# Kernel tuning notes

Hardware: AMD Instinct MI355X
Metric: run time of the kernel (lower is better)

The kernel has to match this reference:

```python
import jax, jax.numpy as jnp
import numpy as np

VAR_NUM = 96
EMBED_TIME = 128
INPUT_DIM = VAR_NUM * 2 + EMBED_TIME  # 320
ATTN_DIM = 64
N_HEADS = 8
ALL_DIM = ATTN_DIM * N_HEADS  # 512
B, N = 8, 2048
NEG_INF = -1e9  # finite stand-in for masked_fill(-inf); safe under softmax


def setup_inputs() -> dict:
    key = jax.random.key(0)
    ks = jax.random.split(key, 16)
    s = lambda d: 1.0 / np.sqrt(d)
    return {
        "times_in": jax.random.uniform(ks[0], (B, N), jnp.float32),
        "data_in": jax.random.normal(ks[1], (B, N, VAR_NUM), jnp.float32),
        "mask_in": jnp.ones((B, N, VAR_NUM), jnp.float32),
        "exist_times": jax.random.randint(ks[2], (B, N), 0, 2, jnp.int32),
        # TimeEmbedding params
        "w_per": jax.random.normal(ks[3], (1, EMBED_TIME - 1), jnp.float32),
        "b_per": jnp.zeros((EMBED_TIME - 1,), jnp.float32),
        "w_lin": jax.random.normal(ks[4], (1, 1), jnp.float32),
        "b_lin": jnp.zeros((1,), jnp.float32),
        # Attention params
        "Wq": jax.random.normal(ks[5], (INPUT_DIM, ALL_DIM), jnp.float32) * s(INPUT_DIM),
        "bq": jnp.zeros((ALL_DIM,), jnp.float32),
        "Wk": jax.random.normal(ks[6], (INPUT_DIM, ALL_DIM), jnp.float32) * s(INPUT_DIM),
        "bk": jnp.zeros((ALL_DIM,), jnp.float32),
        "Wv": jax.random.normal(ks[7], (INPUT_DIM, ALL_DIM), jnp.float32) * s(INPUT_DIM),
        "bv": jnp.zeros((ALL_DIM,), jnp.float32),
        "Wfc": jax.random.normal(ks[8], (ALL_DIM, ATTN_DIM), jnp.float32) * s(ALL_DIM),
        "bfc": jnp.zeros((ATTN_DIM,), jnp.float32),
    }


def reference(times_in, data_in, mask_in, exist_times,
              w_per, b_per, w_lin, b_lin,
              Wq, bq, Wk, bk, Wv, bv, Wfc, bfc):
    b, n = times_in.shape
    tt = times_in[..., None]  # [b, n, 1]
    # TimeEmbedding: [linear(tt), sin(periodic(tt))]
    te = jnp.concatenate([tt @ w_lin + b_lin, jnp.sin(tt @ w_per + b_per)], axis=-1)
    x = jnp.concatenate([data_in, mask_in, te], axis=-1)  # [b, n, INPUT_DIM]

    def heads(w, bias):
        return (x @ w + bias).reshape(b, n, N_HEADS, ATTN_DIM).transpose(0, 2, 1, 3)

    q, k, v = heads(Wq, bq), heads(Wk, bk), heads(Wv, bv)  # [b, h, n, d]
    # NOTE: custom scale uses sqrt(input_dim), not sqrt(head_dim)
    scores = jnp.einsum("bhqd,bhkd->bhqk", q, k) / jnp.sqrt(jnp.float32(INPUT_DIM))
    m = (exist_times != 0)
    scores = jnp.where(m[:, None, None, :], scores, NEG_INF)  # mask keys
    attn = jax.nn.softmax(scores, axis=-1)  # dropout p=0 in eval reference
    out = jnp.einsum("bhqk,bhkd->bhqd", attn, v)
    out = jnp.where(m[:, None, :, None], out, 0.0)  # zero masked query rows
    out = out.transpose(0, 2, 1, 3).reshape(b, n, ALL_DIM)
    return out @ Wfc + bfc  # [b, n, ATTN_DIM]
```

## Files before the change

kernel.cpp:

```cpp
#include <hip/hip_runtime.h>

#define N_ 2048
#define BN 16384
#define IN_DIM 320
#define QKV_N 1536
#define ALPHA 0.08064911f

typedef float f32x4 __attribute__((ext_vector_type(4)));
typedef short v8s __attribute__((ext_vector_type(8)));
typedef unsigned int u32x2 __attribute__((ext_vector_type(2)));

__device__ __forceinline__ short f2b(float f) {
  unsigned u = __builtin_bit_cast(unsigned, f);
  u = u + 0x7fff + ((u >> 16) & 1);
  return (short)(u >> 16);
}

__device__ __forceinline__ int piperm(int t) {
  return ((t >> 5) & 1) * 32 + ((t >> 2) & 3) * 8 + ((t >> 4) & 1) * 4 + (t & 3);
}

__global__ void build_x(const float* __restrict__ times, const float* __restrict__ data,
                        const float* __restrict__ maskv, const float* __restrict__ w_per,
                        const float* __restrict__ b_per, const float* __restrict__ w_lin,
                        const float* __restrict__ b_lin, short* __restrict__ x) {
  int row = blockIdx.x;
  int t = threadIdx.x;
  float tt = times[row];
  short* xr = x + (size_t)row * IN_DIM;
  const float* dr = data + (size_t)row * 96;
  const float* mr = maskv + (size_t)row * 96;
  if (t < 96) { xr[t] = f2b(dr[t]); xr[96 + t] = f2b(mr[t]); }
  float val;
  if (t == 0) val = tt * w_lin[0] + b_lin[0];
  else        val = __sinf(tt * w_per[t - 1] + b_per[t - 1]);
  xr[192 + t] = f2b(val);
}

__global__ void scan_mask(const int* __restrict__ exist, int* __restrict__ prefix,
                          int* __restrict__ ntg, short* __restrict__ flagsc) {
  __shared__ int sums[256];
  int b = blockIdx.x;
  int t = threadIdx.x;
  const int* e = exist + b * 2048;
  int loc[8];
  int s = 0;
#pragma unroll
  for (int j = 0; j < 8; ++j) { loc[j] = s; s += (e[t * 8 + j] != 0) ? 1 : 0; }
  sums[t] = s;
  __syncthreads();
  for (int d = 1; d < 256; d <<= 1) {
    int v = (t >= d) ? sums[t - d] : 0;
    __syncthreads();
    sums[t] += v;
    __syncthreads();
  }
  int total = sums[255];
  int base = (t == 0) ? 0 : sums[t - 1];
#pragma unroll
  for (int j = 0; j < 8; ++j) prefix[b * 2048 + t * 8 + j] = base + loc[j];
  if (t == 0) ntg[b] = (total + 63) >> 6;
#pragma unroll
  for (int j = 0; j < 8; ++j) {
    int slot = t * 8 + j;
    flagsc[b * 2048 + (slot & ~63) + piperm(slot & 63)] =
        (slot < total) ? (short)0x3F80 : (short)0;
  }
}

__global__ void zero_pad(const int* __restrict__ ntg, short* __restrict__ kT,
                         short* __restrict__ vT) {
  int bh = blockIdx.x;
  int nt = ntg[bh >> 3];
  if (nt == 0) return;
  size_t base = (size_t)bh * 131072 + (size_t)(nt - 1) * 4096;
  int t = threadIdx.x;
  v8s z = {0, 0, 0, 0, 0, 0, 0, 0};
  *(v8s*)&kT[base + t * 8] = z;
  *(v8s*)&vT[base + t * 8] = z;
}

__global__ void transpose_w(const float* __restrict__ Wq, const float* __restrict__ Wk,
                            const float* __restrict__ Wv, const float* __restrict__ Wfc,
                            short* __restrict__ Wt, short* __restrict__ WfcT) {
  int idx = blockIdx.x * 256 + threadIdx.x;
  if (idx < QKV_N * IN_DIM) {
    int n = idx / IN_DIM, kk = idx - n * IN_DIM;
    const float* W = (n < 512) ? Wq : (n < 1024 ? Wk : Wv);
    Wt[idx] = f2b(W[(size_t)kk * 512 + (n & 511)]);
  } else {
    int j = idx - QKV_N * IN_DIM;
    int d = j >> 9, kk = j & 511;
    WfcT[j] = f2b(Wfc[kk * 64 + d]);
  }
}

__launch_bounds__(256)
__global__ void qkv_gemm(const short* __restrict__ x, const short* __restrict__ Wt,
                         const float* __restrict__ bq, const float* __restrict__ bk,
                         const float* __restrict__ bv, const int* __restrict__ exist,
                         const int* __restrict__ prefix,
                         short* __restrict__ q, short* __restrict__ kT, short* __restrict__ vT) {
  __shared__ short As[128][40];
  __shared__ short Bs[128][40];
  int bm = blockIdx.x;
  int bn = blockIdx.y;
  int tid = threadIdx.x, wave = tid >> 6, lane = tid & 63;
  int wm = wave >> 1, wn = wave & 1;
  int l16 = lane & 15, lh = lane >> 4;
  f32x4 acc[4][4] = {};
  for (int kt = 0; kt < 10; ++kt) {
    int k0 = kt * 32;
#pragma unroll
    for (int s = 0; s < 2; ++s) {
      int c = tid + s * 256;
      int r = c >> 2, c8 = c & 3;
      *(v8s*)&As[r][c8 * 8] = *(const v8s*)&x[(size_t)(bm * 128 + r) * IN_DIM + k0 + c8 * 8];
      *(v8s*)&Bs[r][c8 * 8] = *(const v8s*)&Wt[(size_t)(bn * 128 + r) * IN_DIM + k0 + c8 * 8];
    }
    __syncthreads();
    v8s af[4], bfr[4];
#pragma unroll
    for (int m = 0; m < 4; ++m) af[m] = *(const v8s*)&As[wm * 64 + m * 16 + l16][lh * 8];
#pragma unroll
    for (int n = 0; n < 4; ++n) bfr[n] = *(const v8s*)&Bs[wn * 64 + n * 16 + l16][lh * 8];
#pragma unroll
    for (int m = 0; m < 4; ++m)
#pragma unroll
      for (int n = 0; n < 4; ++n)
        acc[m][n] = __builtin_amdgcn_mfma_f32_16x16x32_bf16(af[m], bfr[n], acc[m][n], 0, 0, 0);
    __syncthreads();
  }
  int w = bn >> 2;
  if (w == 0) {
#pragma unroll
    for (int m = 0; m < 4; ++m) {
      int row0 = bm * 128 + wm * 64 + m * 16 + lh * 4;
#pragma unroll
      for (int n = 0; n < 4; ++n) {
        int c = (bn * 128 + wn * 64 + n * 16 + l16) & 511;
        float bb = bq[c];
        int h = c >> 6, d = c & 63;
#pragma unroll
        for (int r = 0; r < 4; ++r) {
          int rr = row0 + r;
          int b = rr >> 11, ntok = rr & 2047;
          q[(((size_t)(b * 8 + h) * N_ + ntok) << 6) + d] = f2b((acc[m][n][r] + bb) * ALPHA);
        }
      }
    }
  } else if (w == 1) {
    int b = bm >> 4;
#pragma unroll
    for (int m = 0; m < 4; ++m) {
      int row0 = bm * 128 + wm * 64 + m * 16 + lh * 4;
      int exr[4], dstr[4];
#pragma unroll
      for (int r = 0; r < 4; ++r) { exr[r] = exist[row0 + r]; dstr[r] = prefix[row0 + r]; }
#pragma unroll
      for (int n = 0; n < 4; ++n) {
        int c = (bn * 128 + wn * 64 + n * 16 + l16) & 511;
        float bb = bk[c];
        int h = c >> 6;
        int d = n * 16 + l16;
        int kc2 = d >> 5, lh2 = (d >> 3) & 3, j = d & 7;
        size_t hb = (size_t)(b * 8 + h) * 131072;
#pragma unroll
        for (int r = 0; r < 4; ++r) {
          if (exr[r]) {
            int dst = dstr[r];
            size_t addr = hb + (size_t)(dst >> 6) * 4096
                        + (size_t)((((dst >> 4) & 3) * 2 + kc2) * 512)
                        + lh2 * 128 + (dst & 15) * 8 + j;
            kT[addr] = f2b(acc[m][n][r] + bb);
          }
        }
      }
    }
  } else {
    int b = bm >> 4;
#pragma unroll
    for (int m = 0; m < 4; ++m) {
      int row0 = bm * 128 + wm * 64 + m * 16 + lh * 4;
      int exr[4], dstr[4];
#pragma unroll
      for (int r = 0; r < 4; ++r) { exr[r] = exist[row0 + r]; dstr[r] = prefix[row0 + r]; }
#pragma unroll
      for (int n = 0; n < 4; ++n) {
        int c = (bn * 128 + wn * 64 + n * 16 + l16) & 511;
        float bb = bv[c];
        int h = c >> 6;
        size_t hb = (size_t)(b * 8 + h) * 131072;
#pragma unroll
        for (int r = 0; r < 4; ++r) {
          if (exr[r]) {
            int dst = dstr[r];
            int t2 = dst & 63;
            int jj = ((t2 >> 4) & 1) * 4 + (t2 & 3);
            size_t addr = hb + (size_t)(dst >> 6) * 4096
                        + (size_t)((n * 2 + ((t2 >> 5) & 1)) * 512)
                        + ((t2 >> 2) & 3) * 128 + l16 * 8 + jj;
            vT[addr] = f2b(acc[m][n][r] + bb);
          }
        }
      }
    }
  }
}

__launch_bounds__(256, 2)
__global__ void attn_kernel(const short* __restrict__ q, const short* __restrict__ kT,
                            const short* __restrict__ vT, const short* __restrict__ flagsc,
                            const int* __restrict__ ntg, const int* __restrict__ exist,
                            short* __restrict__ att) {
  int bx = blockIdx.x;
  int bh = ((bx >> 6) << 3) | (bx & 7);
  int qblk = (bx >> 3) & 7;
  int b = bh >> 3, h = bh & 7;
  int tid = threadIdx.x, wave = tid >> 6, lane = tid & 63;
  int l16 = lane & 15, lh = lane >> 4;
  int q0 = qblk * 256 + wave * 64;
  int nt = ntg[b];
  const short* qp = q + (size_t)bh * N_ * 64;
  const short* kpt = kT + (size_t)bh * 131072;
  const short* vpt = vT + (size_t)bh * 131072;
  const short* fpt = flagsc + b * N_;
  const int* ex = exist + b * N_;
  v8s qf[4][2];
#pragma unroll
  for (int m = 0; m < 4; ++m)
#pragma unroll
    for (int kc = 0; kc < 2; ++kc)
      qf[m][kc] = *(const v8s*)&qp[(size_t)(q0 + m * 16 + l16) * 64 + kc * 32 + lh * 8];
  f32x4 oacc[4][4] = {};
  f32x4 lacc[4] = {};
  const f32x4 zf = {0.f, 0.f, 0.f, 0.f};
  int voff = lane * 8;
  v8s kf[8], vf[8], ff[2];
#pragma unroll
  for (int i = 0; i < 8; ++i) {
    kf[i] = *(const v8s*)&kpt[i * 512 + voff];
    vf[i] = *(const v8s*)&vpt[i * 512 + voff];
  }
  ff[0] = *(const v8s*)&fpt[lh * 8];
  ff[1] = *(const v8s*)&fpt[32 + lh * 8];
#pragma unroll 1
  for (int kt = 0; kt < nt; ++kt) {
    const short* kn = kpt + (size_t)(kt + 1) * 4096;
    const short* vn = vpt + (size_t)(kt + 1) * 4096;
    const short* fn = fpt + (kt + 1) * 64;
    bool pre = (kt + 1 < nt);
#pragma unroll
    for (int mh = 0; mh < 2; ++mh) {
      f32x4 sacc[2][4];
#pragma unroll
      for (int n = 0; n < 4; ++n)
#pragma unroll
        for (int mm = 0; mm < 2; ++mm) {
          sacc[mm][n] = __builtin_amdgcn_mfma_f32_16x16x32_bf16(kf[n * 2], qf[mh * 2 + mm][0], zf, 0, 0, 0);
          sacc[mm][n] = __builtin_amdgcn_mfma_f32_16x16x32_bf16(kf[n * 2 + 1], qf[mh * 2 + mm][1], sacc[mm][n], 0, 0, 0);
        }
      if (mh == 1 && pre)
#pragma unroll
        for (int i = 0; i < 8; ++i) kf[i] = *(const v8s*)&kn[i * 512 + voff];
      v8s pf[2][2];
#pragma unroll
      for (int mm = 0; mm < 2; ++mm)
#pragma unroll
        for (int kc = 0; kc < 2; ++kc)
#pragma unroll
          for (int half = 0; half < 2; ++half) {
            int n = kc * 2 + half;
            float p0 = __builtin_amdgcn_exp2f(sacc[mm][n][0]);
            float p1 = __builtin_amdgcn_exp2f(sacc[mm][n][1]);
            float p2 = __builtin_amdgcn_exp2f(sacc[mm][n][2]);
            float p3 = __builtin_amdgcn_exp2f(sacc[mm][n][3]);
            uint w0, w1;
            asm("v_cvt_pk_bf16_f32 %0, %1, %2" : "=v"(w0) : "v"(p0), "v"(p1));
            asm("v_cvt_pk_bf16_f32 %0, %1, %2" : "=v"(w1) : "v"(p2), "v"(p3));
            ((uint*)&pf[mm][kc])[half * 2]     = w0;
            ((uint*)&pf[mm][kc])[half * 2 + 1] = w1;
          }
#pragma unroll
      for (int kc = 0; kc < 2; ++kc) {
#pragma unroll
        for (int mm = 0; mm < 2; ++mm)
          lacc[mh * 2 + mm] = __builtin_amdgcn_mfma_f32_16x16x32_bf16(pf[mm][kc], ff[kc], lacc[mh * 2 + mm], 0, 0, 0);
#pragma unroll
        for (int n = 0; n < 4; ++n)
#pragma unroll
          for (int mm = 0; mm < 2; ++mm)
            oacc[mh * 2 + mm][n] = __builtin_amdgcn_mfma_f32_16x16x32_bf16(pf[mm][kc], vf[n * 2 + kc], oacc[mh * 2 + mm][n], 0, 0, 0);
      }
    }
    if (pre) {
#pragma unroll
      for (int i = 0; i < 8; ++i) vf[i] = *(const v8s*)&vn[i * 512 + voff];
      ff[0] = *(const v8s*)&fn[lh * 8];
      ff[1] = *(const v8s*)&fn[32 + lh * 8];
    }
  }
#pragma unroll
  for (int m = 0; m < 4; ++m)
#pragma unroll
    for (int r = 0; r < 4; ++r) {
      int row = q0 + m * 16 + lh * 4 + r;
      float qm = (ex[row] != 0) ? 1.f : 0.f;
      float inv = qm / fmaxf(lacc[m][r], 1e-20f);
#pragma unroll
      for (int n = 0; n < 4; ++n)
        att[((size_t)(b * N_ + row)) * 512 + h * 64 + n * 16 + l16] = f2b(oacc[m][n][r] * inv);
    }
}

__launch_bounds__(256)
__global__ void out_gemm(const short* __restrict__ att, const short* __restrict__ WfcT,
                         const float* __restrict__ bfc, float* __restrict__ out) {
  __shared__ short As[128][40];
  __shared__ short Bs[64][40];
  int bm = blockIdx.x;
  int tid = threadIdx.x, wave = tid >> 6, lane = tid & 63;
  int l16 = lane & 15, lh = lane >> 4;
  f32x4 acc[2][4] = {};
  for (int kt = 0; kt < 16; ++kt) {
    int k0 = kt * 32;
#pragma unroll
    for (int s = 0; s < 2; ++s) {
      int c = tid + s * 256;
      int r = c >> 2, c8 = c & 3;
      *(v8s*)&As[r][c8 * 8] = *(const v8s*)&att[(size_t)(bm * 128 + r) * 512 + k0 + c8 * 8];
    }
    { int r = tid >> 2, c8 = tid & 3;
      if (r < 64) *(v8s*)&Bs[r][c8 * 8] = *(const v8s*)&WfcT[(size_t)r * 512 + k0 + c8 * 8]; }
    __syncthreads();
    v8s bfr[4];
#pragma unroll
    for (int n = 0; n < 4; ++n) bfr[n] = *(const v8s*)&Bs[n * 16 + l16][lh * 8];
#pragma unroll
    for (int m = 0; m < 2; ++m) {
      v8s af = *(const v8s*)&As[wave * 32 + m * 16 + l16][lh * 8];
#pragma unroll
      for (int n = 0; n < 4; ++n)
        acc[m][n] = __builtin_amdgcn_mfma_f32_16x16x32_bf16(af, bfr[n], acc[m][n], 0, 0, 0);
    }
    __syncthreads();
  }
#pragma unroll
  for (int m = 0; m < 2; ++m)
#pragma unroll
    for (int n = 0; n < 4; ++n) {
      float bb = bfc[n * 16 + l16];
#pragma unroll
      for (int r = 0; r < 4; ++r) {
        int row = bm * 128 + wave * 32 + m * 16 + lh * 4 + r;
        out[(size_t)row * 64 + n * 16 + l16] = acc[m][n][r] + bb;
      }
    }
}

extern "C" void kernel_launch(void* const* d_in, const int* in_sizes, int n_in,
                              void* d_out, int out_size, void* d_ws, size_t ws_size,
                              hipStream_t stream) {
  const float* times = (const float*)d_in[0];
  const float* data  = (const float*)d_in[1];
  const float* maskv = (const float*)d_in[2];
  const int*   exist = (const int*)d_in[3];
  const float* w_per = (const float*)d_in[4];
  const float* b_per = (const float*)d_in[5];
  const float* w_lin = (const float*)d_in[6];
  const float* b_lin = (const float*)d_in[7];
  const float* Wq  = (const float*)d_in[8];
  const float* bq  = (const float*)d_in[9];
  const float* Wk  = (const float*)d_in[10];
  const float* bk  = (const float*)d_in[11];
  const float* Wv  = (const float*)d_in[12];
  const float* bv  = (const float*)d_in[13];
  const float* Wfc = (const float*)d_in[14];
  const float* bfc = (const float*)d_in[15];
  float* out = (float*)d_out;

  char* ws = (char*)d_ws;
  short* x     = (short*)(ws);
  short* Wt    = (short*)(ws + 10485760);
  short* WfcT  = (short*)(ws + 11468800);
  short* qb    = (short*)(ws + 11534336);
  short* kTb   = (short*)(ws + 28311552);
  short* vTb   = (short*)(ws + 45088768);
  short* att   = (short*)(ws + 61865984);
  short* flagsc= (short*)(ws + 78643200);
  int*   prefix= (int*)(ws + 78675968);
  int*   ntg   = (int*)(ws + 78741504);

  build_x<<<BN, 128, 0, stream>>>(times, data, maskv, w_per, b_per, w_lin, b_lin, x);
  scan_mask<<<8, 256, 0, stream>>>(exist, prefix, ntg, flagsc);
  zero_pad<<<64, 512, 0, stream>>>(ntg, kTb, vTb);
  transpose_w<<<2048, 256, 0, stream>>>(Wq, Wk, Wv, Wfc, Wt, WfcT);
  qkv_gemm<<<dim3(128, 12), 256, 0, stream>>>(x, Wt, bq, bk, bv, exist, prefix, qb, kTb, vTb);
  attn_kernel<<<512, 256, 0, stream>>>(qb, kTb, vTb, flagsc, ntg, exist, att);
  out_gemm<<<128, 256, 0, stream>>>(att, WfcT, bfc, out);
}
```

Measured before the change: 109.9 us.

## Write compacted K/V row-major from QKV GEMM and fragmentize V separately

The QKV GEMM epilogue now writes compacted K and V in plain row-major [bh, token, d] layout instead of scattered MFMA-fragment layouts. The attention kernel reads K directly from row-major with per-lane row offsets. A new fragmentize kernel transposes V through shared memory into the fragment layout, and zero_pad now clears only the padded tail rows of K. The goal is more contiguous global stores in the GEMM epilogue, at the cost of an extra kernel launch and an extra pass over V.

```diff
diff --git a/kernel.cpp b/kernel.cpp
--- a/kernel.cpp
+++ b/kernel.cpp
@@ -38,7 +38,8 @@
 }
 
 __global__ void scan_mask(const int* __restrict__ exist, int* __restrict__ prefix,
-                          int* __restrict__ ntg, short* __restrict__ flagsc) {
+                          int* __restrict__ ntg, int* __restrict__ totals,
+                          short* __restrict__ flagsc) {
   __shared__ int sums[256];
   int b = blockIdx.x;
   int t = threadIdx.x;
@@ -59,7 +60,7 @@
   int base = (t == 0) ? 0 : sums[t - 1];
 #pragma unroll
   for (int j = 0; j < 8; ++j) prefix[b * 2048 + t * 8 + j] = base + loc[j];
-  if (t == 0) ntg[b] = (total + 63) >> 6;
+  if (t == 0) { ntg[b] = (total + 63) >> 6; totals[b] = total; }
 #pragma unroll
   for (int j = 0; j < 8; ++j) {
     int slot = t * 8 + j;
@@ -68,16 +69,16 @@
   }
 }
 
-__global__ void zero_pad(const int* __restrict__ ntg, short* __restrict__ kT,
-                         short* __restrict__ vT) {
+__global__ void zero_pad(const int* __restrict__ ntg, const int* __restrict__ totals,
+                         short* __restrict__ kc) {
   int bh = blockIdx.x;
-  int nt = ntg[bh >> 3];
-  if (nt == 0) return;
-  size_t base = (size_t)bh * 131072 + (size_t)(nt - 1) * 4096;
+  int b = bh >> 3;
+  int nt = ntg[b], total = totals[b];
+  int pad = nt * 64 - total;
   int t = threadIdx.x;
   v8s z = {0, 0, 0, 0, 0, 0, 0, 0};
-  *(v8s*)&kT[base + t * 8] = z;
-  *(v8s*)&vT[base + t * 8] = z;
+  for (int i = t; i < pad * 8; i += 512)
+    *(v8s*)&kc[((size_t)bh * N_ + total) * 64 + i * 8] = z;
 }
 
 __global__ void transpose_w(const float* __restrict__ Wq, const float* __restrict__ Wk,
@@ -100,7 +101,7 @@
                          const float* __restrict__ bq, const float* __restrict__ bk,
                          const float* __restrict__ bv, const int* __restrict__ exist,
                          const int* __restrict__ prefix,
-                         short* __restrict__ q, short* __restrict__ kT, short* __restrict__ vT) {
+                         short* __restrict__ q, short* __restrict__ kc, short* __restrict__ vc) {
   __shared__ short As[128][40];
   __shared__ short Bs[128][40];
   int bm = blockIdx.x;
@@ -149,67 +150,69 @@
         }
       }
     }
-  } else if (w == 1) {
-    int b = bm >> 4;
+  } else {
+    short* dbuf = (w == 1) ? kc : vc;
+    const float* bias = (w == 1) ? bk : bv;
 #pragma unroll
     for (int m = 0; m < 4; ++m) {
       int row0 = bm * 128 + wm * 64 + m * 16 + lh * 4;
       int exr[4], dstr[4];
 #pragma unroll
       for (int r = 0; r < 4; ++r) { exr[r] = exist[row0 + r]; dstr[r] = prefix[row0 + r]; }
+      int b = row0 >> 11;
 #pragma unroll
       for (int n = 0; n < 4; ++n) {
         int c = (bn * 128 + wn * 64 + n * 16 + l16) & 511;
-        float bb = bk[c];
-        int h = c >> 6;
-        int d = n * 16 + l16;
-        int kc2 = d >> 5, lh2 = (d >> 3) & 3, j = d & 7;
-        size_t hb = (size_t)(b * 8 + h) * 131072;
-#pragma unroll
-        for (int r = 0; r < 4; ++r) {
-          if (exr[r]) {
-            int dst = dstr[r];
-            size_t addr = hb + (size_t)(dst >> 6) * 4096
-                        + (size_t)((((dst >> 4) & 3) * 2 + kc2) * 512)
-                        + lh2 * 128 + (dst & 15) * 8 + j;
-            kT[addr] = f2b(acc[m][n][r] + bb);
-          }
-        }
+        float bb = bias[c];
+        int h = c >> 6, d = c & 63;
+#pragma unroll
+        for (int r = 0; r < 4; ++r)
+          if (exr[r])
+            dbuf[(((size_t)(b * 8 + h) * N_ + dstr[r]) << 6) + d] = f2b(acc[m][n][r] + bb);
       }
     }
-  } else {
-    int b = bm >> 4;
-#pragma unroll
-    for (int m = 0; m < 4; ++m) {
-      int row0 = bm * 128 + wm * 64 + m * 16 + lh * 4;
-      int exr[4], dstr[4];
-#pragma unroll
-      for (int r = 0; r < 4; ++r) { exr[r] = exist[row0 + r]; dstr[r] = prefix[row0 + r]; }
-#pragma unroll
-      for (int n = 0; n < 4; ++n) {
-        int c = (bn * 128 + wn * 64 + n * 16 + l16) & 511;
-        float bb = bv[c];
-        int h = c >> 6;
-        size_t hb = (size_t)(b * 8 + h) * 131072;
-#pragma unroll
-        for (int r = 0; r < 4; ++r) {
-          if (exr[r]) {
-            int dst = dstr[r];
-            int t2 = dst & 63;
-            int jj = ((t2 >> 4) & 1) * 4 + (t2 & 3);
-            size_t addr = hb + (size_t)(dst >> 6) * 4096
-                        + (size_t)((n * 2 + ((t2 >> 5) & 1)) * 512)
-                        + ((t2 >> 2) & 3) * 128 + l16 * 8 + jj;
-            vT[addr] = f2b(acc[m][n][r] + bb);
-          }
-        }
+  }
+}
+
+__launch_bounds__(256)
+__global__ void fragmentize(const short* __restrict__ vc, const int* __restrict__ ntg,
+                            const int* __restrict__ totals, short* __restrict__ vT) {
+  __shared__ short Vs[64][66];
+  int bh = blockIdx.x;
+  int b = bh >> 3;
+  int nt = ntg[b], total = totals[b];
+  int tid = threadIdx.x;
+  const short* vcp = vc + (size_t)bh * N_ * 64;
+  short* vtp = vT + (size_t)bh * 131072;
+  for (int tile = blockIdx.y; tile < nt; tile += 4) {
+    int base = tile * 64;
+#pragma unroll
+    for (int s = 0; s < 2; ++s) {
+      int c = tid + s * 256, r = c >> 3, c8 = c & 7;
+      v8s val = {0, 0, 0, 0, 0, 0, 0, 0};
+      if (base + r < total) val = *(const v8s*)&vcp[(size_t)(base + r) * 64 + c8 * 8];
+      *(v8s*)&Vs[r][c8 * 8] = val;
+    }
+    __syncthreads();
+#pragma unroll
+    for (int s = 0; s < 2; ++s) {
+      int c = tid + s * 256;
+      int l16 = c & 15, lh = (c >> 4) & 3, kc2 = (c >> 6) & 1, n2 = c >> 7;
+      int d = n2 * 16 + l16;
+      v8s o;
+#pragma unroll
+      for (int jj = 0; jj < 8; ++jj) {
+        int t2 = kc2 * 32 + (jj >> 2) * 16 + lh * 4 + (jj & 3);
+        o[jj] = Vs[t2][d];
       }
-    }
+      *(v8s*)&vtp[(size_t)tile * 4096 + c * 8] = o;
+    }
+    __syncthreads();
   }
 }
 
 __launch_bounds__(256, 2)
-__global__ void attn_kernel(const short* __restrict__ q, const short* __restrict__ kT,
+__global__ void attn_kernel(const short* __restrict__ q, const short* __restrict__ kc,
                             const short* __restrict__ vT, const short* __restrict__ flagsc,
                             const int* __restrict__ ntg, const int* __restrict__ exist,
                             short* __restrict__ att) {
@@ -222,7 +225,7 @@
   int q0 = qblk * 256 + wave * 64;
   int nt = ntg[b];
   const short* qp = q + (size_t)bh * N_ * 64;
-  const short* kpt = kT + (size_t)bh * 131072;
+  const short* kcp = kc + (size_t)bh * N_ * 64;
   const short* vpt = vT + (size_t)bh * 131072;
   const short* fpt = flagsc + b * N_;
   const int* ex = exist + b * N_;
@@ -230,23 +233,24 @@
 #pragma unroll
   for (int m = 0; m < 4; ++m)
 #pragma unroll
-    for (int kc = 0; kc < 2; ++kc)
-      qf[m][kc] = *(const v8s*)&qp[(size_t)(q0 + m * 16 + l16) * 64 + kc * 32 + lh * 8];
+    for (int kcx = 0; kcx < 2; ++kcx)
+      qf[m][kcx] = *(const v8s*)&qp[(size_t)(q0 + m * 16 + l16) * 64 + kcx * 32 + lh * 8];
   f32x4 oacc[4][4] = {};
   f32x4 lacc[4] = {};
   const f32x4 zf = {0.f, 0.f, 0.f, 0.f};
   int voff = lane * 8;
+  int vok = l16 * 64 + lh * 8;
   v8s kf[8], vf[8], ff[2];
 #pragma unroll
   for (int i = 0; i < 8; ++i) {
-    kf[i] = *(const v8s*)&kpt[i * 512 + voff];
+    kf[i] = *(const v8s*)&kcp[(i >> 1) * 1024 + (i & 1) * 32 + vok];
     vf[i] = *(const v8s*)&vpt[i * 512 + voff];
   }
   ff[0] = *(const v8s*)&fpt[lh * 8];
   ff[1] = *(const v8s*)&fpt[32 + lh * 8];
 #pragma unroll 1
   for (int kt = 0; kt < nt; ++kt) {
-    const short* kn = kpt + (size_t)(kt + 1) * 4096;
+    const short* kn = kcp + (size_t)(kt + 1) * 4096;
     const short* vn = vpt + (size_t)(kt + 1) * 4096;
     const short* fn = fpt + (kt + 1) * 64;
     bool pre = (kt + 1 < nt);
@@ -262,15 +266,16 @@
         }
       if (mh == 1 && pre)
 #pragma unroll
-        for (int i = 0; i < 8; ++i) kf[i] = *(const v8s*)&kn[i * 512 + voff];
+        for (int i = 0; i < 8; ++i)
+          kf[i] = *(const v8s*)&kn[(i >> 1) * 1024 + (i & 1) * 32 + vok];
       v8s pf[2][2];
 #pragma unroll
       for (int mm = 0; mm < 2; ++mm)
 #pragma unroll
-        for (int kc = 0; kc < 2; ++kc)
+        for (int kcx = 0; kcx < 2; ++kcx)
 #pragma unroll
           for (int half = 0; half < 2; ++half) {
-            int n = kc * 2 + half;
+            int n = kcx * 2 + half;
             float p0 = __builtin_amdgcn_exp2f(sacc[mm][n][0]);
             float p1 = __builtin_amdgcn_exp2f(sacc[mm][n][1]);
             float p2 = __builtin_amdgcn_exp2f(sacc[mm][n][2]);
@@ -278,19 +283,19 @@
             uint w0, w1;
             asm("v_cvt_pk_bf16_f32 %0, %1, %2" : "=v"(w0) : "v"(p0), "v"(p1));
             asm("v_cvt_pk_bf16_f32 %0, %1, %2" : "=v"(w1) : "v"(p2), "v"(p3));
-            ((uint*)&pf[mm][kc])[half * 2]     = w0;
-            ((uint*)&pf[mm][kc])[half * 2 + 1] = w1;
+            ((uint*)&pf[mm][kcx])[half * 2]     = w0;
+            ((uint*)&pf[mm][kcx])[half * 2 + 1] = w1;
           }
 #pragma unroll
-      for (int kc = 0; kc < 2; ++kc) {
+      for (int kcx = 0; kcx < 2; ++kcx) {
 #pragma unroll
         for (int mm = 0; mm < 2; ++mm)
-          lacc[mh * 2 + mm] = __builtin_amdgcn_mfma_f32_16x16x32_bf16(pf[mm][kc], ff[kc], lacc[mh * 2 + mm], 0, 0, 0);
+          lacc[mh * 2 + mm] = __builtin_amdgcn_mfma_f32_16x16x32_bf16(pf[mm][kcx], ff[kcx], lacc[mh * 2 + mm], 0, 0, 0);
 #pragma unroll
         for (int n = 0; n < 4; ++n)
 #pragma unroll
           for (int mm = 0; mm < 2; ++mm)
-            oacc[mh * 2 + mm][n] = __builtin_amdgcn_mfma_f32_16x16x32_bf16(pf[mm][kc], vf[n * 2 + kc], oacc[mh * 2 + mm][n], 0, 0, 0);
+            oacc[mh * 2 + mm][n] = __builtin_amdgcn_mfma_f32_16x16x32_bf16(pf[mm][kcx], vf[n * 2 + kcx], oacc[mh * 2 + mm][n], 0, 0, 0);
       }
     }
     if (pre) {
@@ -384,18 +389,21 @@
   short* Wt    = (short*)(ws + 10485760);
   short* WfcT  = (short*)(ws + 11468800);
   short* qb    = (short*)(ws + 11534336);
-  short* kTb   = (short*)(ws + 28311552);
+  short* kcb   = (short*)(ws + 28311552);
   short* vTb   = (short*)(ws + 45088768);
+  short* vcb   = (short*)(ws + 61865984);
   short* att   = (short*)(ws + 61865984);
   short* flagsc= (short*)(ws + 78643200);
   int*   prefix= (int*)(ws + 78675968);
   int*   ntg   = (int*)(ws + 78741504);
+  int*   totals= (int*)(ws + 78741536);
 
   build_x<<<BN, 128, 0, stream>>>(times, data, maskv, w_per, b_per, w_lin, b_lin, x);
-  scan_mask<<<8, 256, 0, stream>>>(exist, prefix, ntg, flagsc);
-  zero_pad<<<64, 512, 0, stream>>>(ntg, kTb, vTb);
+  scan_mask<<<8, 256, 0, stream>>>(exist, prefix, ntg, totals, flagsc);
   transpose_w<<<2048, 256, 0, stream>>>(Wq, Wk, Wv, Wfc, Wt, WfcT);
-  qkv_gemm<<<dim3(128, 12), 256, 0, stream>>>(x, Wt, bq, bk, bv, exist, prefix, qb, kTb, vTb);
-  attn_kernel<<<512, 256, 0, stream>>>(qb, kTb, vTb, flagsc, ntg, exist, att);
+  qkv_gemm<<<dim3(128, 12), 256, 0, stream>>>(x, Wt, bq, bk, bv, exist, prefix, qb, kcb, vcb);
+  zero_pad<<<64, 512, 0, stream>>>(ntg, totals, kcb);
+  fragmentize<<<dim3(64, 4), 256, 0, stream>>>(vcb, ntg, totals, vTb);
+  attn_kernel<<<512, 256, 0, stream>>>(qb, kcb, vTb, flagsc, ntg, exist, att);
   out_gemm<<<128, 256, 0, stream>>>(att, WfcT, bfc, out);
 }
```

Result: slower. 126.8 us (+15.3%).
